# Optimization experiments

Measured on AMD Instinct MI355X. Metric: run time of the kernel, lower is better.

Reference implementation:

```python
import jax, jax.numpy as jnp
import numpy as np


def setup_inputs() -> dict:
    key = jax.random.key(0)
    k1, k2, k3 = jax.random.split(key, 3)
    B, N, D = 64, 2048, 1024
    output = jax.random.normal(k1, (B, 1, D), dtype=jnp.float32)
    context = jax.random.normal(k2, (B, N, D), dtype=jnp.float32)
    # nn.Linear(2*dim, dim): weight [dim, 2*dim], bias [dim]
    W_out = jax.random.normal(k3, (D, 2 * D), dtype=jnp.float32) * (1.0 / np.sqrt(2 * D))
    b_out = jnp.zeros((D,), dtype=jnp.float32)
    return {"output": output, "context": context, "W_out": W_out, "b_out": b_out}


def reference(output, context, W_out, b_out):
    B, q, D = output.shape  # q == 1
    N = context.shape[1]
    # scores: (B, q, N) = output @ context^T
    attn = jnp.einsum('bqd,bnd->bqn', output, context)
    attn = jax.nn.softmax(attn, axis=-1)
    # mix: (B, q, D)
    mix = jnp.einsum('bqn,bnd->bqd', attn, context)
    combined = jnp.concatenate([mix, output], axis=-1)  # (B, q, 2D)
    out = jnp.tanh(jnp.einsum('bqe,de->bqd', combined, W_out) + b_out)
    return (out, attn)
```

## Files before the change

kernel.cpp:

```cpp
#include <hip/hip_runtime.h>
#include <cmath>

#define BATCH 64
#define NCTX 2048
#define DIM 1024
#define CHUNKS 32
#define ROWS_PER_CHUNK (NCTX / CHUNKS)
#define ROWS_PER_WAVE (ROWS_PER_CHUNK / 4)

__global__ __launch_bounds__(256) void attn_phase1(
    const float* __restrict__ q,
    const float* __restrict__ ctx,
    float* __restrict__ scores,
    float* __restrict__ part_m,
    float* __restrict__ part_l,
    float* __restrict__ part_o)
{
    const int blk  = blockIdx.x;
    const int b    = blk / CHUNKS;
    const int c    = blk % CHUNKS;
    const int tid  = threadIdx.x;
    const int wave = tid >> 6;
    const int lane = tid & 63;

    float4 qf[4];
    const float* qb = q + (size_t)b * DIM;
    #pragma unroll
    for (int j = 0; j < 4; ++j)
        qf[j] = *reinterpret_cast<const float4*>(qb + lane * 4 + 256 * j);

    float m = -INFINITY, l = 0.f;
    float4 o[4];
    #pragma unroll
    for (int j = 0; j < 4; ++j) o[j] = make_float4(0.f, 0.f, 0.f, 0.f);

    const int row0 = c * ROWS_PER_CHUNK + wave * ROWS_PER_WAVE;
    const float* cb = ctx + (size_t)b * NCTX * DIM;
    float* sc = scores + (size_t)b * NCTX;

    for (int i = 0; i < ROWS_PER_WAVE; i += 2) {
        const int rowA = row0 + i;
        const int rowB = rowA + 1;
        const float* crA = cb + (size_t)rowA * DIM + lane * 4;
        const float* crB = cb + (size_t)rowB * DIM + lane * 4;
        float4 cfA[4], cfB[4];
        #pragma unroll
        for (int j = 0; j < 4; ++j) {
            cfA[j] = *reinterpret_cast<const float4*>(crA + 256 * j);
            cfB[j] = *reinterpret_cast<const float4*>(crB + 256 * j);
        }

        float dA[4], dB[4];
        #pragma unroll
        for (int j = 0; j < 4; ++j) {
            dA[j] = qf[j].x * cfA[j].x + qf[j].y * cfA[j].y
                  + qf[j].z * cfA[j].z + qf[j].w * cfA[j].w;
            dB[j] = qf[j].x * cfB[j].x + qf[j].y * cfB[j].y
                  + qf[j].z * cfB[j].z + qf[j].w * cfB[j].w;
        }
        float s0 = (dA[0] + dA[1]) + (dA[2] + dA[3]);
        float s1 = (dB[0] + dB[1]) + (dB[2] + dB[3]);

        #pragma unroll
        for (int off = 32; off >= 1; off >>= 1) {
            s0 += __shfl_xor(s0, off, 64);
            s1 += __shfl_xor(s1, off, 64);
        }

        if (lane < 2) sc[rowA + lane] = lane ? s1 : s0;

        const float m_new = fmaxf(m, fmaxf(s0, s1));
        if (m_new > m) {
            const float a = __expf(m - m_new);
            l *= a;
            #pragma unroll
            for (int j = 0; j < 4; ++j) {
                o[j].x *= a; o[j].y *= a; o[j].z *= a; o[j].w *= a;
            }
            m = m_new;
        }
        const float p0 = __expf(s0 - m);
        const float p1 = __expf(s1 - m);
        l += p0 + p1;
        #pragma unroll
        for (int j = 0; j < 4; ++j) {
            o[j].x += p0 * cfA[j].x + p1 * cfB[j].x;
            o[j].y += p0 * cfA[j].y + p1 * cfB[j].y;
            o[j].z += p0 * cfA[j].z + p1 * cfB[j].z;
            o[j].w += p0 * cfA[j].w + p1 * cfB[j].w;
        }
    }

    __shared__ float wm[4], wl[4];
    __shared__ float o_lds[4 * DIM];
    if (lane == 0) { wm[wave] = m; wl[wave] = l; }
    __syncthreads();

    const float Mb = fmaxf(fmaxf(wm[0], wm[1]), fmaxf(wm[2], wm[3]));
    float Lb = 0.f;
    #pragma unroll
    for (int w = 0; w < 4; ++w) Lb += wl[w] * __expf(wm[w] - Mb);

    const float aw = __expf(m - Mb);
    #pragma unroll
    for (int j = 0; j < 4; ++j) {
        float4 t = o[j];
        t.x *= aw; t.y *= aw; t.z *= aw; t.w *= aw;
        *reinterpret_cast<float4*>(&o_lds[wave * DIM + lane * 4 + 256 * j]) = t;
    }
    __syncthreads();

    {
        const int e = tid * 4;
        float4 s0 = *reinterpret_cast<const float4*>(&o_lds[0 * DIM + e]);
        float4 s1 = *reinterpret_cast<const float4*>(&o_lds[1 * DIM + e]);
        float4 s2 = *reinterpret_cast<const float4*>(&o_lds[2 * DIM + e]);
        float4 s3 = *reinterpret_cast<const float4*>(&o_lds[3 * DIM + e]);
        float4 r;
        r.x = s0.x + s1.x + s2.x + s3.x;
        r.y = s0.y + s1.y + s2.y + s3.y;
        r.z = s0.z + s1.z + s2.z + s3.z;
        r.w = s0.w + s1.w + s2.w + s3.w;
        *reinterpret_cast<float4*>(&part_o[((size_t)b * CHUNKS + c) * DIM + e]) = r;
    }
    if (tid == 0) {
        part_m[b * CHUNKS + c] = Mb;
        part_l[b * CHUNKS + c] = Lb;
    }
}

__global__ __launch_bounds__(256) void attn_phase2(
    const float* __restrict__ scores,
    const float* __restrict__ part_m,
    const float* __restrict__ part_l,
    const float* __restrict__ part_o,
    float* __restrict__ mix,
    float* __restrict__ attn_out)
{
    const int b = blockIdx.x;
    const int tid = threadIdx.x;

    float M = -INFINITY;
    #pragma unroll
    for (int i = 0; i < CHUNKS; ++i) M = fmaxf(M, part_m[b * CHUNKS + i]);

    float w[CHUNKS];
    float L = 0.f;
    #pragma unroll
    for (int i = 0; i < CHUNKS; ++i) {
        w[i] = __expf(part_m[b * CHUNKS + i] - M);
        L += part_l[b * CHUNKS + i] * w[i];
    }
    const float invL = 1.f / L;

    const int e = tid * 4;
    float4 acc = make_float4(0.f, 0.f, 0.f, 0.f);
    #pragma unroll
    for (int i = 0; i < CHUNKS; ++i) {
        float4 t = *reinterpret_cast<const float4*>(
            &part_o[((size_t)b * CHUNKS + i) * DIM + e]);
        acc.x += t.x * w[i];
        acc.y += t.y * w[i];
        acc.z += t.z * w[i];
        acc.w += t.w * w[i];
    }
    acc.x *= invL; acc.y *= invL; acc.z *= invL; acc.w *= invL;
    *reinterpret_cast<float4*>(&mix[(size_t)b * DIM + e]) = acc;

    for (int n = tid; n < NCTX; n += 256)
        attn_out[(size_t)b * NCTX + n] =
            __expf(scores[(size_t)b * NCTX + n] - M) * invL;
}

#define BT 4
#define DT 32
__global__ __launch_bounds__(256) void attn_phase3(
    const float* __restrict__ mix,
    const float* __restrict__ q,
    const float* __restrict__ W,
    const float* __restrict__ bias,
    float* __restrict__ out)
{
    const int d_chunk = blockIdx.x % (DIM / DT);
    const int b_chunk = blockIdx.x / (DIM / DT);
    const int d0 = d_chunk * DT;
    const int b0 = b_chunk * BT;
    const int tid  = threadIdx.x;
    const int wave = tid >> 6;
    const int lane = tid & 63;

    __shared__ float comb[BT * 2 * DIM];
    for (int i = tid; i < BT * 2 * DIM; i += 256) {
        const int bl = i >> 11;
        const int e  = i & 2047;
        comb[i] = (e < DIM) ? mix[(size_t)(b0 + bl) * DIM + e]
                            : q[(size_t)(b0 + bl) * DIM + (e - DIM)];
    }
    __syncthreads();

    const int d_base = d0 + wave * (DT / 4);
    #pragma unroll
    for (int g = 0; g < 2; ++g) {
        const int dg = d_base + g * 4;
        float acc[4][BT];
        #pragma unroll
        for (int di = 0; di < 4; ++di)
            #pragma unroll
            for (int bl = 0; bl < BT; ++bl) acc[di][bl] = 0.f;

        for (int kk = 0; kk < 2 * DIM; kk += 256) {
            float4 wv[4];
            #pragma unroll
            for (int di = 0; di < 4; ++di)
                wv[di] = *reinterpret_cast<const float4*>(
                    W + (size_t)(dg + di) * (2 * DIM) + kk + lane * 4);
            #pragma unroll
            for (int bl = 0; bl < BT; ++bl) {
                float4 cv = *reinterpret_cast<const float4*>(
                    &comb[bl * 2 * DIM + kk + lane * 4]);
                #pragma unroll
                for (int di = 0; di < 4; ++di) {
                    acc[di][bl] += wv[di].x * cv.x;
                    acc[di][bl] += wv[di].y * cv.y;
                    acc[di][bl] += wv[di].z * cv.z;
                    acc[di][bl] += wv[di].w * cv.w;
                }
            }
        }

        float myval = 0.f;
        #pragma unroll
        for (int di = 0; di < 4; ++di) {
            #pragma unroll
            for (int bl = 0; bl < BT; ++bl) {
                float v = acc[di][bl];
                #pragma unroll
                for (int off = 32; off >= 1; off >>= 1)
                    v += __shfl_xor(v, off, 64);
                if (lane == di * BT + bl) myval = v;
            }
        }
        if (lane < 16) {
            const int di = lane >> 2;
            const int bl = lane & 3;
            const int d  = dg + di;
            out[(size_t)(b0 + bl) * DIM + d] = tanhf(myval + bias[d]);
        }
    }
}

extern "C" void kernel_launch(void* const* d_in, const int* in_sizes, int n_in,
                              void* d_out, int out_size, void* d_ws, size_t ws_size,
                              hipStream_t stream) {
    const float* q    = (const float*)d_in[0];
    const float* ctx  = (const float*)d_in[1];
    const float* W    = (const float*)d_in[2];
    const float* bias = (const float*)d_in[3];

    float* out_main = (float*)d_out;
    float* attn_out = (float*)d_out + (size_t)BATCH * DIM;

    float* ws      = (float*)d_ws;
    float* scores  = ws;
    float* part_m  = scores + (size_t)BATCH * NCTX;
    float* part_l  = part_m + BATCH * CHUNKS;
    float* part_o  = part_l + BATCH * CHUNKS;
    float* mix     = part_o + (size_t)BATCH * CHUNKS * DIM;

    attn_phase1<<<BATCH * CHUNKS, 256, 0, stream>>>(q, ctx, scores,
                                                    part_m, part_l, part_o);
    attn_phase2<<<BATCH, 256, 0, stream>>>(scores, part_m, part_l, part_o,
                                           mix, attn_out);
    attn_phase3<<<(DIM / DT) * (BATCH / BT), 256, 0, stream>>>(mix, q, W, bias,
                                                               out_main);
}
```

Before: 711.2 us.

## Unroll context rows by four, use nontemporal loads, halve chunks, split phase2

The phase1 loop now processes four context rows per iteration with nontemporal vector loads, aiming for more memory-level parallelism on the 512MB context stream and less cache pollution. The chunk count drops from 32 to 16, which halves the partial outputs phase2 must reduce, at the cost of fewer blocks in phase1. Phase2 is split across four blocks per batch to spread the reduction and the attention normalization. The extra registers for four rows may lower occupancy.

Measured after the change: 675.1 us. 5.1% less time.

```diff
diff --git a/kernel.cpp b/kernel.cpp
--- a/kernel.cpp
+++ b/kernel.cpp
@@ -4,9 +4,11 @@
 #define BATCH 64
 #define NCTX 2048
 #define DIM 1024
-#define CHUNKS 32
+#define CHUNKS 16
 #define ROWS_PER_CHUNK (NCTX / CHUNKS)
 #define ROWS_PER_WAVE (ROWS_PER_CHUNK / 4)
+
+typedef float f4_t __attribute__((ext_vector_type(4)));
 
 __global__ __launch_bounds__(256) void attn_phase1(
     const float* __restrict__ q,
@@ -23,71 +25,84 @@
     const int wave = tid >> 6;
     const int lane = tid & 63;
 
-    float4 qf[4];
+    f4_t qf[4];
     const float* qb = q + (size_t)b * DIM;
     #pragma unroll
     for (int j = 0; j < 4; ++j)
-        qf[j] = *reinterpret_cast<const float4*>(qb + lane * 4 + 256 * j);
+        qf[j] = *reinterpret_cast<const f4_t*>(qb + lane * 4 + 256 * j);
 
     float m = -INFINITY, l = 0.f;
-    float4 o[4];
-    #pragma unroll
-    for (int j = 0; j < 4; ++j) o[j] = make_float4(0.f, 0.f, 0.f, 0.f);
+    f4_t o[4];
+    #pragma unroll
+    for (int j = 0; j < 4; ++j) o[j] = (f4_t)(0.f);
 
     const int row0 = c * ROWS_PER_CHUNK + wave * ROWS_PER_WAVE;
     const float* cb = ctx + (size_t)b * NCTX * DIM;
     float* sc = scores + (size_t)b * NCTX;
 
-    for (int i = 0; i < ROWS_PER_WAVE; i += 2) {
-        const int rowA = row0 + i;
-        const int rowB = rowA + 1;
-        const float* crA = cb + (size_t)rowA * DIM + lane * 4;
-        const float* crB = cb + (size_t)rowB * DIM + lane * 4;
-        float4 cfA[4], cfB[4];
-        #pragma unroll
-        for (int j = 0; j < 4; ++j) {
-            cfA[j] = *reinterpret_cast<const float4*>(crA + 256 * j);
-            cfB[j] = *reinterpret_cast<const float4*>(crB + 256 * j);
-        }
-
-        float dA[4], dB[4];
-        #pragma unroll
-        for (int j = 0; j < 4; ++j) {
-            dA[j] = qf[j].x * cfA[j].x + qf[j].y * cfA[j].y
-                  + qf[j].z * cfA[j].z + qf[j].w * cfA[j].w;
-            dB[j] = qf[j].x * cfB[j].x + qf[j].y * cfB[j].y
-                  + qf[j].z * cfB[j].z + qf[j].w * cfB[j].w;
-        }
-        float s0 = (dA[0] + dA[1]) + (dA[2] + dA[3]);
-        float s1 = (dB[0] + dB[1]) + (dB[2] + dB[3]);
+    for (int i = 0; i < ROWS_PER_WAVE; i += 4) {
+        f4_t cf[4][4];
+        #pragma unroll
+        for (int r = 0; r < 4; ++r) {
+            const float* cr = cb + (size_t)(row0 + i + r) * DIM + lane * 4;
+            #pragma unroll
+            for (int j = 0; j < 4; ++j)
+                cf[r][j] = __builtin_nontemporal_load(
+                    reinterpret_cast<const f4_t*>(cr + 256 * j));
+        }
+
+        float s[4];
+        #pragma unroll
+        for (int r = 0; r < 4; ++r) {
+            float d0 = qf[0].x * cf[r][0].x + qf[0].y * cf[r][0].y
+                     + qf[0].z * cf[r][0].z + qf[0].w * cf[r][0].w;
+            float d1 = qf[1].x * cf[r][1].x + qf[1].y * cf[r][1].y
+                     + qf[1].z * cf[r][1].z + qf[1].w * cf[r][1].w;
+            float d2 = qf[2].x * cf[r][2].x + qf[2].y * cf[r][2].y
+                     + qf[2].z * cf[r][2].z + qf[2].w * cf[r][2].w;
+            float d3 = qf[3].x * cf[r][3].x + qf[3].y * cf[r][3].y
+                     + qf[3].z * cf[r][3].z + qf[3].w * cf[r][3].w;
+            s[r] = (d0 + d1) + (d2 + d3);
+        }
 
         #pragma unroll
         for (int off = 32; off >= 1; off >>= 1) {
-            s0 += __shfl_xor(s0, off, 64);
-            s1 += __shfl_xor(s1, off, 64);
-        }
-
-        if (lane < 2) sc[rowA + lane] = lane ? s1 : s0;
-
-        const float m_new = fmaxf(m, fmaxf(s0, s1));
+            s[0] += __shfl_xor(s[0], off, 64);
+            s[1] += __shfl_xor(s[1], off, 64);
+            s[2] += __shfl_xor(s[2], off, 64);
+            s[3] += __shfl_xor(s[3], off, 64);
+        }
+
+        {
+            float sv = (lane == 1) ? s[1] : (lane == 2) ? s[2]
+                     : (lane == 3) ? s[3] : s[0];
+            if (lane < 4) sc[row0 + i + lane] = sv;
+        }
+
+        const float mx = fmaxf(fmaxf(s[0], s[1]), fmaxf(s[2], s[3]));
+        const float m_new = fmaxf(m, mx);
         if (m_new > m) {
             const float a = __expf(m - m_new);
             l *= a;
             #pragma unroll
-            for (int j = 0; j < 4; ++j) {
-                o[j].x *= a; o[j].y *= a; o[j].z *= a; o[j].w *= a;
-            }
+            for (int j = 0; j < 4; ++j) o[j] *= a;
             m = m_new;
         }
-        const float p0 = __expf(s0 - m);
-        const float p1 = __expf(s1 - m);
-        l += p0 + p1;
+        const float p0 = __expf(s[0] - m);
+        const float p1 = __expf(s[1] - m);
+        const float p2 = __expf(s[2] - m);
+        const float p3 = __expf(s[3] - m);
+        l += (p0 + p1) + (p2 + p3);
         #pragma unroll
         for (int j = 0; j < 4; ++j) {
-            o[j].x += p0 * cfA[j].x + p1 * cfB[j].x;
-            o[j].y += p0 * cfA[j].y + p1 * cfB[j].y;
-            o[j].z += p0 * cfA[j].z + p1 * cfB[j].z;
-            o[j].w += p0 * cfA[j].w + p1 * cfB[j].w;
+            o[j].x += p0 * cf[0][j].x + p1 * cf[1][j].x
+                    + p2 * cf[2][j].x + p3 * cf[3][j].x;
+            o[j].y += p0 * cf[0][j].y + p1 * cf[1][j].y
+                    + p2 * cf[2][j].y + p3 * cf[3][j].y;
+            o[j].z += p0 * cf[0][j].z + p1 * cf[1][j].z
+                    + p2 * cf[2][j].z + p3 * cf[3][j].z;
+            o[j].w += p0 * cf[0][j].w + p1 * cf[1][j].w
+                    + p2 * cf[2][j].w + p3 * cf[3][j].w;
         }
     }
 
@@ -104,24 +119,19 @@
     const float aw = __expf(m - Mb);
     #pragma unroll
     for (int j = 0; j < 4; ++j) {
-        float4 t = o[j];
-        t.x *= aw; t.y *= aw; t.z *= aw; t.w *= aw;
-        *reinterpret_cast<float4*>(&o_lds[wave * DIM + lane * 4 + 256 * j]) = t;
+        f4_t t = o[j] * aw;
+        *reinterpret_cast<f4_t*>(&o_lds[wave * DIM + lane * 4 + 256 * j]) = t;
     }
     __syncthreads();
 
     {
         const int e = tid * 4;
-        float4 s0 = *reinterpret_cast<const float4*>(&o_lds[0 * DIM + e]);
-        float4 s1 = *reinterpret_cast<const float4*>(&o_lds[1 * DIM + e]);
-        float4 s2 = *reinterpret_cast<const float4*>(&o_lds[2 * DIM + e]);
-        float4 s3 = *reinterpret_cast<const float4*>(&o_lds[3 * DIM + e]);
-        float4 r;
-        r.x = s0.x + s1.x + s2.x + s3.x;
-        r.y = s0.y + s1.y + s2.y + s3.y;
-        r.z = s0.z + s1.z + s2.z + s3.z;
-        r.w = s0.w + s1.w + s2.w + s3.w;
-        *reinterpret_cast<float4*>(&part_o[((size_t)b * CHUNKS + c) * DIM + e]) = r;
+        f4_t s0 = *reinterpret_cast<const f4_t*>(&o_lds[0 * DIM + e]);
+        f4_t s1 = *reinterpret_cast<const f4_t*>(&o_lds[1 * DIM + e]);
+        f4_t s2 = *reinterpret_cast<const f4_t*>(&o_lds[2 * DIM + e]);
+        f4_t s3 = *reinterpret_cast<const f4_t*>(&o_lds[3 * DIM + e]);
+        f4_t r = (s0 + s1) + (s2 + s3);
+        *reinterpret_cast<f4_t*>(&part_o[((size_t)b * CHUNKS + c) * DIM + e]) = r;
     }
     if (tid == 0) {
         part_m[b * CHUNKS + c] = Mb;
@@ -137,8 +147,9 @@
     float* __restrict__ mix,
     float* __restrict__ attn_out)
 {
-    const int b = blockIdx.x;
-    const int tid = threadIdx.x;
+    const int b    = blockIdx.x >> 2;
+    const int part = blockIdx.x & 3;
+    const int tid  = threadIdx.x;
 
     float M = -INFINITY;
     #pragma unroll
@@ -153,23 +164,21 @@
     }
     const float invL = 1.f / L;
 
-    const int e = tid * 4;
-    float4 acc = make_float4(0.f, 0.f, 0.f, 0.f);
-    #pragma unroll
-    for (int i = 0; i < CHUNKS; ++i) {
-        float4 t = *reinterpret_cast<const float4*>(
-            &part_o[((size_t)b * CHUNKS + i) * DIM + e]);
-        acc.x += t.x * w[i];
-        acc.y += t.y * w[i];
-        acc.z += t.z * w[i];
-        acc.w += t.w * w[i];
-    }
-    acc.x *= invL; acc.y *= invL; acc.z *= invL; acc.w *= invL;
-    *reinterpret_cast<float4*>(&mix[(size_t)b * DIM + e]) = acc;
-
-    for (int n = tid; n < NCTX; n += 256)
+    {
+        const int e = part * 256 + tid;
+        float acc = 0.f;
+        #pragma unroll
+        for (int i = 0; i < CHUNKS; ++i)
+            acc += part_o[((size_t)b * CHUNKS + i) * DIM + e] * w[i];
+        mix[(size_t)b * DIM + e] = acc * invL;
+    }
+
+    #pragma unroll
+    for (int t = 0; t < 2; ++t) {
+        const int n = part * 512 + t * 256 + tid;
         attn_out[(size_t)b * NCTX + n] =
             __expf(scores[(size_t)b * NCTX + n] - M) * invL;
+    }
 }
 
 #define BT 4
@@ -209,14 +218,14 @@
             for (int bl = 0; bl < BT; ++bl) acc[di][bl] = 0.f;
 
         for (int kk = 0; kk < 2 * DIM; kk += 256) {
-            float4 wv[4];
+            f4_t wv[4];
             #pragma unroll
             for (int di = 0; di < 4; ++di)
-                wv[di] = *reinterpret_cast<const float4*>(
+                wv[di] = *reinterpret_cast<const f4_t*>(
                     W + (size_t)(dg + di) * (2 * DIM) + kk + lane * 4);
             #pragma unroll
             for (int bl = 0; bl < BT; ++bl) {
-                float4 cv = *reinterpret_cast<const float4*>(
+                f4_t cv = *reinterpret_cast<const f4_t*>(
                     &comb[bl * 2 * DIM + kk + lane * 4]);
                 #pragma unroll
                 for (int di = 0; di < 4; ++di) {
@@ -269,8 +278,8 @@
 
     attn_phase1<<<BATCH * CHUNKS, 256, 0, stream>>>(q, ctx, scores,
                                                     part_m, part_l, part_o);
-    attn_phase2<<<BATCH, 256, 0, stream>>>(scores, part_m, part_l, part_o,
-                                           mix, attn_out);
+    attn_phase2<<<BATCH * 4, 256, 0, stream>>>(scores, part_m, part_l, part_o,
+                                               mix, attn_out);
     attn_phase3<<<(DIM / DT) * (BATCH / BT), 256, 0, stream>>>(mix, q, W, bias,
                                                                out_main);
 }
```
